# Kernel optimization log

Hardware: AMD Instinct MI355X
Metric: run time of the kernel (lower is better)

The kernel has to match this reference:

```python
import jax, jax.numpy as jnp
import numpy as np

B, S, H, I, E, TOPK = 2, 2048, 1024, 2816, 7, 2


def setup_inputs() -> dict:
    key = jax.random.key(0)
    ks = jax.random.split(key, 8)
    sh = 1.0 / np.sqrt(H).astype(np.float32)   # fan-in scale for H->I projections
    si = 1.0 / np.sqrt(I).astype(np.float32)   # fan-in scale for I->H projections
    return {
        "x": jax.random.normal(ks[0], (B, S, H), jnp.float32),
        "Wg_shared": jax.random.normal(ks[1], (I, H), jnp.float32) * sh,
        "Wu_shared": jax.random.normal(ks[2], (I, H), jnp.float32) * sh,
        "Wd_shared": jax.random.normal(ks[3], (H, I), jnp.float32) * si,
        "Wg": jax.random.normal(ks[4], (E, I, H), jnp.float32) * sh,
        "Wu": jax.random.normal(ks[5], (E, I, H), jnp.float32) * sh,
        "Wd": jax.random.normal(ks[6], (E, H, I), jnp.float32) * si,
        "Wr": jax.random.normal(ks[7], (E, H), jnp.float32) * sh,
    }


def reference(x, Wg_shared, Wu_shared, Wd_shared, Wg, Wu, Wd, Wr):
    # Shared expert: SwiGLU MLP applied to every token.
    sg = jnp.einsum('bsh,ih->bsi', x, Wg_shared)
    su = jnp.einsum('bsh,ih->bsi', x, Wu_shared)
    shared_out = jnp.einsum('bsi,hi->bsh', jax.nn.silu(sg) * su, Wd_shared)

    # Router: top-k over logits, softmax over the selected k logits.
    router_logits = jnp.einsum('bsh,eh->bse', x, Wr)          # [B,S,E]
    rw, sel = jax.lax.top_k(router_logits, TOPK)              # [B,S,K]
    rw = jax.nn.softmax(rw, axis=-1)
    # Per-expert combine weight (equivalent to the scatter-built mask * weight).
    comb = jnp.sum(rw[..., None] * jax.nn.one_hot(sel, E, dtype=x.dtype), axis=2)  # [B,S,E]

    # Torch module runs every expert densely on every token, then masks.
    g = jnp.einsum('bsh,eih->ebsi', x, Wg)                    # [E,B,S,I]
    u = jnp.einsum('bsh,eih->ebsi', x, Wu)
    y = jnp.einsum('ebsi,ehi->ebsh', jax.nn.silu(g) * u, Wd)  # [E,B,S,H]
    moe_out = jnp.einsum('ebsh,bse->bsh', y, comb)

    return shared_out + moe_out, router_logits
```

## Files before the change

kernel.cpp:

```cpp
#include <hip/hip_runtime.h>
#include <hip/hip_bf16.h>

#define NTOK 4096
#define HH 1024
#define II 2816
#define EE 7
#define SHARED_BASE 8192
#define NSLOT 12288

typedef __bf16 bf16x8 __attribute__((ext_vector_type(8)));
typedef __bf16 bf16x4 __attribute__((ext_vector_type(4)));
typedef float  f32x4v __attribute__((ext_vector_type(4)));

__global__ void cvt_x(const float* __restrict__ x, __bf16* __restrict__ xb) {
    int i = blockIdx.x * blockDim.x + threadIdx.x;
    const f32x4v* xv = (const f32x4v*)x;
    bf16x4* ov = (bf16x4*)xb;
    int base = i * 4;
#pragma unroll
    for (int j = 0; j < 4; j++) {
        f32x4v f = xv[base + j];
        bf16x4 b;
        b[0] = (__bf16)f[0]; b[1] = (__bf16)f[1];
        b[2] = (__bf16)f[2]; b[3] = (__bf16)f[3];
        ov[base + j] = b;
    }
}

__global__ void router_k(const float* __restrict__ x, const float* __restrict__ Wr,
                         float* __restrict__ logits, int* __restrict__ counts,
                         int* __restrict__ sel, float* __restrict__ wtop,
                         int* __restrict__ tlist, float* __restrict__ wlist) {
    int wave = threadIdx.x >> 6;
    int lane = threadIdx.x & 63;
    int t = blockIdx.x * 4 + wave;
    const float* xr = x + (size_t)t * HH;
    double acc[EE];
#pragma unroll
    for (int e = 0; e < EE; e++) acc[e] = 0.0;
    for (int j = 0; j < 16; j++) {
        int h = lane + j * 64;
        double xv = (double)xr[h];
#pragma unroll
        for (int e = 0; e < EE; e++) acc[e] += xv * (double)Wr[e * HH + h];
    }
#pragma unroll
    for (int e = 0; e < EE; e++) {
        for (int off = 32; off > 0; off >>= 1) acc[e] += __shfl_down(acc[e], off, 64);
    }
    if (lane == 0) {
        int e0 = 0;
        for (int e = 1; e < EE; e++) if (acc[e] > acc[e0]) e0 = e;
        int e1 = -1;
        for (int e = 0; e < EE; e++) {
            if (e == e0) continue;
            if (e1 < 0 || acc[e] > acc[e1]) e1 = e;
        }
        double w1 = exp(acc[e1] - acc[e0]);
        double s = 1.0 + w1;
        for (int e = 0; e < EE; e++) logits[(size_t)t * EE + e] = (float)acc[e];
        sel[2 * t] = e0; sel[2 * t + 1] = e1;
        wtop[2 * t] = (float)(1.0 / s); wtop[2 * t + 1] = (float)(w1 / s);
        atomicAdd(&counts[e0], 1);
        atomicAdd(&counts[e1], 1);
        tlist[SHARED_BASE + t] = t;
        wlist[SHARED_BASE + t] = 1.0f;
    }
}

__global__ void finalize_k(const int* __restrict__ counts, int* __restrict__ cursor,
                           int* __restrict__ nlist, int* __restrict__ offs) {
    if (threadIdx.x == 0 && blockIdx.x == 0) {
        int o = 0;
        for (int e = 0; e < EE; e++) {
            offs[e] = o; cursor[e] = o; nlist[e] = counts[e];
            o += counts[e];
        }
        offs[EE] = SHARED_BASE;
        nlist[EE] = NTOK;
        cursor[EE] = SHARED_BASE;
    }
}

__global__ void scatter_k(const int* __restrict__ sel, const float* __restrict__ wtop,
                          int* __restrict__ cursor, int* __restrict__ tlist,
                          float* __restrict__ wlist) {
    int t = blockIdx.x * blockDim.x + threadIdx.x;
    if (t >= NTOK) return;
#pragma unroll
    for (int j = 0; j < 2; j++) {
        int e = sel[2 * t + j];
        int slot = atomicAdd(&cursor[e], 1);
        tlist[slot] = t;
        wlist[slot] = wtop[2 * t + j];
    }
}

__global__ __launch_bounds__(256, 3) void gateup_k(
        const float* __restrict__ Wg, const float* __restrict__ Wu,
        const float* __restrict__ Wgs, const float* __restrict__ Wus,
        const __bf16* __restrict__ xb, __bf16* __restrict__ hbuf,
        const int* __restrict__ nlist, const int* __restrict__ offs,
        const int* __restrict__ tlist) {
    const int e = blockIdx.z;
    const int ne = nlist[e];
    const int bx = blockIdx.x;
    const int nt = (bx & 7) + 8 * (bx >> 8);
    const int mt = (bx >> 3) & 31;
    if (nt >= II / 64) return;
    if (mt * 128 >= ne) return;
    const int base = offs[e];
    const float* wg = (e < EE) ? Wg + (size_t)e * II * HH : Wgs;
    const float* wu = (e < EE) ? Wu + (size_t)e * II * HH : Wus;

    __shared__ __bf16 As[128 * 32];
    __shared__ __bf16 Bg[64 * 32];
    __shared__ __bf16 Bu[64 * 32];

    const int tid = threadIdx.x;
    const int arow0 = tid >> 2, c8 = (tid & 3) * 8;
    const int arow1 = arow0 + 64;
    const int cl0 = min(mt * 128 + arow0, ne - 1);
    const int cl1 = min(mt * 128 + arow1, ne - 1);
    const __bf16* aptr0 = xb + (size_t)tlist[base + cl0] * HH + c8;
    const __bf16* aptr1 = xb + (size_t)tlist[base + cl1] * HH + c8;
    const int brow = tid >> 2;
    const size_t boff = (size_t)(nt * 64 + brow) * HH + c8;

    const int wid = tid >> 6, lane = tid & 63;
    const int wm = wid >> 1, wn = wid & 1;
    const int l16 = lane & 15, quad = lane >> 4;

    f32x4v accg[4][2], accu[4][2];
#pragma unroll
    for (int i = 0; i < 4; i++)
#pragma unroll
        for (int j = 0; j < 2; j++) { accg[i][j] = (f32x4v)0.0f; accu[i][j] = (f32x4v)0.0f; }

    bf16x8 aR0 = *(const bf16x8*)aptr0;
    bf16x8 aR1 = *(const bf16x8*)aptr1;
    f32x4v g0 = *(const f32x4v*)(wg + boff);
    f32x4v g1 = *(const f32x4v*)(wg + boff + 4);
    f32x4v u0 = *(const f32x4v*)(wu + boff);
    f32x4v u1 = *(const f32x4v*)(wu + boff + 4);

    for (int k0 = 0; k0 < HH; k0 += 32) {
        bf16x8 bgv, buv;
        bgv[0] = (__bf16)g0[0]; bgv[1] = (__bf16)g0[1]; bgv[2] = (__bf16)g0[2]; bgv[3] = (__bf16)g0[3];
        bgv[4] = (__bf16)g1[0]; bgv[5] = (__bf16)g1[1]; bgv[6] = (__bf16)g1[2]; bgv[7] = (__bf16)g1[3];
        buv[0] = (__bf16)u0[0]; buv[1] = (__bf16)u0[1]; buv[2] = (__bf16)u0[2]; buv[3] = (__bf16)u0[3];
        buv[4] = (__bf16)u1[0]; buv[5] = (__bf16)u1[1]; buv[6] = (__bf16)u1[2]; buv[7] = (__bf16)u1[3];
        __syncthreads();
        *(bf16x8*)&As[arow0 * 32 + c8] = aR0;
        *(bf16x8*)&As[arow1 * 32 + c8] = aR1;
        *(bf16x8*)&Bg[brow * 32 + c8] = bgv;
        *(bf16x8*)&Bu[brow * 32 + c8] = buv;
        if (k0 + 32 < HH) {
            aR0 = *(const bf16x8*)(aptr0 + k0 + 32);
            aR1 = *(const bf16x8*)(aptr1 + k0 + 32);
            g0 = *(const f32x4v*)(wg + boff + k0 + 32);
            g1 = *(const f32x4v*)(wg + boff + k0 + 36);
            u0 = *(const f32x4v*)(wu + boff + k0 + 32);
            u1 = *(const f32x4v*)(wu + boff + k0 + 36);
        }
        __syncthreads();
        bf16x8 a[4];
#pragma unroll
        for (int i = 0; i < 4; i++)
            a[i] = *(const bf16x8*)&As[(wm * 64 + i * 16 + l16) * 32 + quad * 8];
#pragma unroll
        for (int j = 0; j < 2; j++) {
            bf16x8 bg = *(const bf16x8*)&Bg[(wn * 32 + j * 16 + l16) * 32 + quad * 8];
            bf16x8 bu = *(const bf16x8*)&Bu[(wn * 32 + j * 16 + l16) * 32 + quad * 8];
#pragma unroll
            for (int i = 0; i < 4; i++) {
                accg[i][j] = __builtin_amdgcn_mfma_f32_16x16x32_bf16(a[i], bg, accg[i][j], 0, 0, 0);
                accu[i][j] = __builtin_amdgcn_mfma_f32_16x16x32_bf16(a[i], bu, accu[i][j], 0, 0, 0);
            }
        }
    }
#pragma unroll
    for (int i = 0; i < 4; i++) {
        const int mrow = mt * 128 + wm * 64 + i * 16 + quad * 4;
#pragma unroll
        for (int r = 0; r < 4; r++) {
            const int slot = mrow + r;
            if (slot < ne) {
                __bf16* hrow = hbuf + (size_t)(base + slot) * II + nt * 64 + wn * 32 + l16;
#pragma unroll
                for (int j = 0; j < 2; j++) {
                    float g = accg[i][j][r], u = accu[i][j][r];
                    float sgl = g / (1.0f + __expf(-g));
                    hrow[j * 16] = (__bf16)(sgl * u);
                }
            }
        }
    }
}

__global__ __launch_bounds__(256, 3) void down_k(
        const float* __restrict__ Wd, const float* __restrict__ Wds,
        const __bf16* __restrict__ hbuf, float* __restrict__ out,
        const int* __restrict__ nlist, const int* __restrict__ offs,
        const int* __restrict__ tlist, const float* __restrict__ wlist) {
    const int e = blockIdx.z;
    const int ne = nlist[e];
    const int bx = blockIdx.x;
    const int nt = bx & 7;
    const int mt = bx >> 3;
    if (mt * 128 >= ne) return;
    const int base = offs[e];
    const float* wd = (e < EE) ? Wd + (size_t)e * HH * II : Wds;

    __shared__ __bf16 As[128 * 32];
    __shared__ __bf16 Bs[128 * 32];

    const int tid = threadIdx.x;
    const int arow0 = tid >> 2, c8 = (tid & 3) * 8;
    const int arow1 = arow0 + 64;
    const int cl0 = min(mt * 128 + arow0, ne - 1);
    const int cl1 = min(mt * 128 + arow1, ne - 1);
    const __bf16* aptr0 = hbuf + (size_t)(base + cl0) * II + c8;
    const __bf16* aptr1 = hbuf + (size_t)(base + cl1) * II + c8;
    const size_t boff0 = (size_t)(nt * 128 + arow0) * II + c8;
    const size_t boff1 = (size_t)(nt * 128 + arow1) * II + c8;

    const int wid = tid >> 6, lane = tid & 63;
    const int wm = wid >> 1, wn = wid & 1;
    const int l16 = lane & 15, quad = lane >> 4;

    f32x4v acc[4][4];
#pragma unroll
    for (int i = 0; i < 4; i++)
#pragma unroll
        for (int j = 0; j < 4; j++) acc[i][j] = (f32x4v)0.0f;

    bf16x8 aR0 = *(const bf16x8*)aptr0;
    bf16x8 aR1 = *(const bf16x8*)aptr1;
    f32x4v b00 = *(const f32x4v*)(wd + boff0);
    f32x4v b01 = *(const f32x4v*)(wd + boff0 + 4);
    f32x4v b10 = *(const f32x4v*)(wd + boff1);
    f32x4v b11 = *(const f32x4v*)(wd + boff1 + 4);

    for (int k0 = 0; k0 < II; k0 += 32) {
        bf16x8 bs0, bs1;
        bs0[0] = (__bf16)b00[0]; bs0[1] = (__bf16)b00[1]; bs0[2] = (__bf16)b00[2]; bs0[3] = (__bf16)b00[3];
        bs0[4] = (__bf16)b01[0]; bs0[5] = (__bf16)b01[1]; bs0[6] = (__bf16)b01[2]; bs0[7] = (__bf16)b01[3];
        bs1[0] = (__bf16)b10[0]; bs1[1] = (__bf16)b10[1]; bs1[2] = (__bf16)b10[2]; bs1[3] = (__bf16)b10[3];
        bs1[4] = (__bf16)b11[0]; bs1[5] = (__bf16)b11[1]; bs1[6] = (__bf16)b11[2]; bs1[7] = (__bf16)b11[3];
        __syncthreads();
        *(bf16x8*)&As[arow0 * 32 + c8] = aR0;
        *(bf16x8*)&As[arow1 * 32 + c8] = aR1;
        *(bf16x8*)&Bs[arow0 * 32 + c8] = bs0;
        *(bf16x8*)&Bs[arow1 * 32 + c8] = bs1;
        if (k0 + 32 < II) {
            aR0 = *(const bf16x8*)(aptr0 + k0 + 32);
            aR1 = *(const bf16x8*)(aptr1 + k0 + 32);
            b00 = *(const f32x4v*)(wd + boff0 + k0 + 32);
            b01 = *(const f32x4v*)(wd + boff0 + k0 + 36);
            b10 = *(const f32x4v*)(wd + boff1 + k0 + 32);
            b11 = *(const f32x4v*)(wd + boff1 + k0 + 36);
        }
        __syncthreads();
        bf16x8 a[4];
#pragma unroll
        for (int i = 0; i < 4; i++)
            a[i] = *(const bf16x8*)&As[(wm * 64 + i * 16 + l16) * 32 + quad * 8];
#pragma unroll
        for (int j = 0; j < 4; j++) {
            bf16x8 b = *(const bf16x8*)&Bs[(wn * 64 + j * 16 + l16) * 32 + quad * 8];
#pragma unroll
            for (int i = 0; i < 4; i++)
                acc[i][j] = __builtin_amdgcn_mfma_f32_16x16x32_bf16(a[i], b, acc[i][j], 0, 0, 0);
        }
    }
#pragma unroll
    for (int i = 0; i < 4; i++) {
        const int mrow = mt * 128 + wm * 64 + i * 16 + quad * 4;
#pragma unroll
        for (int r = 0; r < 4; r++) {
            const int slot = mrow + r;
            if (slot < ne) {
                const int idx = base + slot;
                const int tok = tlist[idx];
                const float w = wlist[idx];
                float* orow = out + (size_t)tok * HH + nt * 128 + wn * 64 + l16;
#pragma unroll
                for (int j = 0; j < 4; j++)
                    atomicAdd(&orow[j * 16], w * acc[i][j][r]);
            }
        }
    }
}

extern "C" void kernel_launch(void* const* d_in, const int* in_sizes, int n_in,
                              void* d_out, int out_size, void* d_ws, size_t ws_size,
                              hipStream_t stream) {
    const float* x   = (const float*)d_in[0];
    const float* Wgs = (const float*)d_in[1];
    const float* Wus = (const float*)d_in[2];
    const float* Wds = (const float*)d_in[3];
    const float* Wg  = (const float*)d_in[4];
    const float* Wu  = (const float*)d_in[5];
    const float* Wd  = (const float*)d_in[6];
    const float* Wr  = (const float*)d_in[7];
    float* out = (float*)d_out;
    float* logits = out + (size_t)NTOK * HH;

    char* ws = (char*)d_ws;
    __bf16* hbuf = (__bf16*)ws;
    __bf16* xb   = (__bf16*)(ws + (size_t)NSLOT * II * 2);
    char* meta   = ws + (size_t)NSLOT * II * 2 + (size_t)NTOK * HH * 2;
    int* counts = (int*)meta;
    int* cursor = counts + 8;
    int* nlist  = cursor + 8;
    int* offs   = nlist + 8;
    int* sel    = offs + 8;
    int* tlist  = sel + 2 * NTOK;
    float* wtop = (float*)(tlist + NSLOT);
    float* wlist = wtop + 2 * NTOK;

    hipMemsetAsync(counts, 0, 8 * sizeof(int), stream);
    hipMemsetAsync(out, 0, (size_t)NTOK * HH * sizeof(float), stream);

    cvt_x<<<1024, 256, 0, stream>>>(x, xb);
    router_k<<<NTOK / 4, 256, 0, stream>>>(x, Wr, logits, counts, sel, wtop, tlist, wlist);
    finalize_k<<<1, 64, 0, stream>>>(counts, cursor, nlist, offs);
    scatter_k<<<NTOK / 256, 256, 0, stream>>>(sel, wtop, cursor, tlist, wlist);
    gateup_k<<<dim3(1536, 1, EE + 1), 256, 0, stream>>>(Wg, Wu, Wgs, Wus, xb, hbuf,
                                                        nlist, offs, tlist);
    down_k<<<dim3(256, 1, EE + 1), 256, 0, stream>>>(Wd, Wds, hbuf, out,
                                                     nlist, offs, tlist, wlist);
}
```

Before: 821.0 us.

## Pre-convert expert weights to bf16 and stream tiles into LDS directly

Adds a kernel that converts all expert and shared gate, up and down weights from fp32 to bf16 into the workspace on every call. New gate/up and down GEMM kernels then load bf16 tiles straight into swizzled LDS with global_load_lds, skipping per-tile fp32 loads and register conversion. Each weight tile is fetched by many token tiles, so halving its bytes should cut repeated fp32 traffic. The cost is an extra full read and write pass over roughly 280 MB of weights per call, and the fast path runs only when the workspace is large enough, otherwise the old fp32 kernels are used.

```diff
diff --git a/kernel.cpp b/kernel.cpp
--- a/kernel.cpp
+++ b/kernel.cpp
@@ -12,6 +12,12 @@
 typedef __bf16 bf16x4 __attribute__((ext_vector_type(4)));
 typedef float  f32x4v __attribute__((ext_vector_type(4)));
 
+typedef const __attribute__((address_space(1))) void* gas_ptr;
+typedef __attribute__((address_space(3))) void* las_ptr;
+__device__ __forceinline__ void load16_lds(const void* g, void* l) {
+    __builtin_amdgcn_global_load_lds((gas_ptr)g, (las_ptr)l, 16, 0, 0);
+}
+
 __global__ void cvt_x(const float* __restrict__ x, __bf16* __restrict__ xb) {
     int i = blockIdx.x * blockDim.x + threadIdx.x;
     const f32x4v* xv = (const f32x4v*)x;
@@ -24,6 +30,32 @@
         b[0] = (__bf16)f[0]; b[1] = (__bf16)f[1];
         b[2] = (__bf16)f[2]; b[3] = (__bf16)f[3];
         ov[base + j] = b;
+    }
+}
+
+__global__ void cvt_w6(const float* __restrict__ s0, const float* __restrict__ s1,
+                       const float* __restrict__ s2, const float* __restrict__ s3,
+                       const float* __restrict__ s4, const float* __restrict__ s5,
+                       __bf16* __restrict__ d0, __bf16* __restrict__ d1,
+                       __bf16* __restrict__ d2, __bf16* __restrict__ d3,
+                       __bf16* __restrict__ d4, __bf16* __restrict__ d5) {
+    const int y = blockIdx.y;
+    const float* s; __bf16* d; int n4;
+    if (y == 0)      { s = s0; d = d0; n4 = (EE * II * HH) / 4; }
+    else if (y == 1) { s = s1; d = d1; n4 = (EE * II * HH) / 4; }
+    else if (y == 2) { s = s2; d = d2; n4 = (EE * II * HH) / 4; }
+    else if (y == 3) { s = s3; d = d3; n4 = (II * HH) / 4; }
+    else if (y == 4) { s = s4; d = d4; n4 = (II * HH) / 4; }
+    else             { s = s5; d = d5; n4 = (II * HH) / 4; }
+    const f32x4v* sv = (const f32x4v*)s;
+    bf16x4* dv = (bf16x4*)d;
+    for (int i = blockIdx.x * blockDim.x + threadIdx.x; i < n4;
+         i += gridDim.x * blockDim.x) {
+        f32x4v f = sv[i];
+        bf16x4 b;
+        b[0] = (__bf16)f[0]; b[1] = (__bf16)f[1];
+        b[2] = (__bf16)f[2]; b[3] = (__bf16)f[3];
+        dv[i] = b;
     }
 }
 
@@ -96,7 +128,176 @@
     }
 }
 
-__global__ __launch_bounds__(256, 3) void gateup_k(
+__global__ __launch_bounds__(256, 3) void gateup_bf(
+        const __bf16* __restrict__ Wg, const __bf16* __restrict__ Wu,
+        const __bf16* __restrict__ Wgs, const __bf16* __restrict__ Wus,
+        const __bf16* __restrict__ xb, __bf16* __restrict__ hbuf,
+        const int* __restrict__ nlist, const int* __restrict__ offs,
+        const int* __restrict__ tlist) {
+    const int e = blockIdx.z;
+    const int ne = nlist[e];
+    const int bx = blockIdx.x;
+    const int nt = (bx & 7) + 8 * (bx >> 8);
+    const int mt = (bx >> 3) & 31;
+    if (nt >= II / 64) return;
+    if (mt * 128 >= ne) return;
+    const int base = offs[e];
+    const __bf16* wg = (e < EE) ? Wg + (size_t)e * II * HH : Wgs;
+    const __bf16* wu = (e < EE) ? Wu + (size_t)e * II * HH : Wus;
+
+    __shared__ __bf16 As[128 * 32];
+    __shared__ __bf16 Bg[64 * 32];
+    __shared__ __bf16 Bu[64 * 32];
+
+    const int tid = threadIdx.x;
+    const int r0 = tid >> 2;
+    const int c  = tid & 3;
+    const int cs = (c ^ ((r0 >> 1) & 3)) * 8;
+    const int cl0 = min(mt * 128 + r0, ne - 1);
+    const int cl1 = min(mt * 128 + r0 + 64, ne - 1);
+    const __bf16* aptr0 = xb + (size_t)tlist[base + cl0] * HH + cs;
+    const __bf16* aptr1 = xb + (size_t)tlist[base + cl1] * HH + cs;
+    const __bf16* bgp = wg + (size_t)(nt * 64 + r0) * HH + cs;
+    const __bf16* bup = wu + (size_t)(nt * 64 + r0) * HH + cs;
+    __bf16* ldsA0 = &As[tid * 8];
+    __bf16* ldsA1 = &As[64 * 32 + tid * 8];
+    __bf16* ldsBg = &Bg[tid * 8];
+    __bf16* ldsBu = &Bu[tid * 8];
+
+    const int wid = tid >> 6, lane = tid & 63;
+    const int wm = wid >> 1, wn = wid & 1;
+    const int l16 = lane & 15, quad = lane >> 4;
+    const int qsw = (quad ^ ((l16 >> 1) & 3)) * 8;
+
+    f32x4v accg[4][2], accu[4][2];
+#pragma unroll
+    for (int i = 0; i < 4; i++)
+#pragma unroll
+        for (int j = 0; j < 2; j++) { accg[i][j] = (f32x4v)0.0f; accu[i][j] = (f32x4v)0.0f; }
+
+    for (int k0 = 0; k0 < HH; k0 += 32) {
+        __syncthreads();
+        load16_lds(aptr0 + k0, ldsA0);
+        load16_lds(aptr1 + k0, ldsA1);
+        load16_lds(bgp + k0, ldsBg);
+        load16_lds(bup + k0, ldsBu);
+        __syncthreads();
+        bf16x8 a[4];
+#pragma unroll
+        for (int i = 0; i < 4; i++)
+            a[i] = *(const bf16x8*)&As[(wm * 64 + i * 16 + l16) * 32 + qsw];
+#pragma unroll
+        for (int j = 0; j < 2; j++) {
+            bf16x8 bg = *(const bf16x8*)&Bg[(wn * 32 + j * 16 + l16) * 32 + qsw];
+            bf16x8 bu = *(const bf16x8*)&Bu[(wn * 32 + j * 16 + l16) * 32 + qsw];
+#pragma unroll
+            for (int i = 0; i < 4; i++) {
+                accg[i][j] = __builtin_amdgcn_mfma_f32_16x16x32_bf16(a[i], bg, accg[i][j], 0, 0, 0);
+                accu[i][j] = __builtin_amdgcn_mfma_f32_16x16x32_bf16(a[i], bu, accu[i][j], 0, 0, 0);
+            }
+        }
+    }
+#pragma unroll
+    for (int i = 0; i < 4; i++) {
+        const int mrow = mt * 128 + wm * 64 + i * 16 + quad * 4;
+#pragma unroll
+        for (int r = 0; r < 4; r++) {
+            const int slot = mrow + r;
+            if (slot < ne) {
+                __bf16* hrow = hbuf + (size_t)(base + slot) * II + nt * 64 + wn * 32 + l16;
+#pragma unroll
+                for (int j = 0; j < 2; j++) {
+                    float g = accg[i][j][r], u = accu[i][j][r];
+                    float sgl = g / (1.0f + __expf(-g));
+                    hrow[j * 16] = (__bf16)(sgl * u);
+                }
+            }
+        }
+    }
+}
+
+__global__ __launch_bounds__(256, 3) void down_bf(
+        const __bf16* __restrict__ Wd, const __bf16* __restrict__ Wds,
+        const __bf16* __restrict__ hbuf, float* __restrict__ out,
+        const int* __restrict__ nlist, const int* __restrict__ offs,
+        const int* __restrict__ tlist, const float* __restrict__ wlist) {
+    const int e = blockIdx.z;
+    const int ne = nlist[e];
+    const int bx = blockIdx.x;
+    const int nt = bx & 7;
+    const int mt = bx >> 3;
+    if (mt * 128 >= ne) return;
+    const int base = offs[e];
+    const __bf16* wd = (e < EE) ? Wd + (size_t)e * HH * II : Wds;
+
+    __shared__ __bf16 As[128 * 32];
+    __shared__ __bf16 Bs[128 * 32];
+
+    const int tid = threadIdx.x;
+    const int r0 = tid >> 2;
+    const int c  = tid & 3;
+    const int cs = (c ^ ((r0 >> 1) & 3)) * 8;
+    const int cl0 = min(mt * 128 + r0, ne - 1);
+    const int cl1 = min(mt * 128 + r0 + 64, ne - 1);
+    const __bf16* aptr0 = hbuf + (size_t)(base + cl0) * II + cs;
+    const __bf16* aptr1 = hbuf + (size_t)(base + cl1) * II + cs;
+    const __bf16* bptr0 = wd + (size_t)(nt * 128 + r0) * II + cs;
+    const __bf16* bptr1 = wd + (size_t)(nt * 128 + r0 + 64) * II + cs;
+    __bf16* ldsA0 = &As[tid * 8];
+    __bf16* ldsA1 = &As[64 * 32 + tid * 8];
+    __bf16* ldsB0 = &Bs[tid * 8];
+    __bf16* ldsB1 = &Bs[64 * 32 + tid * 8];
+
+    const int wid = tid >> 6, lane = tid & 63;
+    const int wm = wid >> 1, wn = wid & 1;
+    const int l16 = lane & 15, quad = lane >> 4;
+    const int qsw = (quad ^ ((l16 >> 1) & 3)) * 8;
+
+    f32x4v acc[4][4];
+#pragma unroll
+    for (int i = 0; i < 4; i++)
+#pragma unroll
+        for (int j = 0; j < 4; j++) acc[i][j] = (f32x4v)0.0f;
+
+    for (int k0 = 0; k0 < II; k0 += 32) {
+        __syncthreads();
+        load16_lds(aptr0 + k0, ldsA0);
+        load16_lds(aptr1 + k0, ldsA1);
+        load16_lds(bptr0 + k0, ldsB0);
+        load16_lds(bptr1 + k0, ldsB1);
+        __syncthreads();
+        bf16x8 a[4];
+#pragma unroll
+        for (int i = 0; i < 4; i++)
+            a[i] = *(const bf16x8*)&As[(wm * 64 + i * 16 + l16) * 32 + qsw];
+#pragma unroll
+        for (int j = 0; j < 4; j++) {
+            bf16x8 b = *(const bf16x8*)&Bs[(wn * 64 + j * 16 + l16) * 32 + qsw];
+#pragma unroll
+            for (int i = 0; i < 4; i++)
+                acc[i][j] = __builtin_amdgcn_mfma_f32_16x16x32_bf16(a[i], b, acc[i][j], 0, 0, 0);
+        }
+    }
+#pragma unroll
+    for (int i = 0; i < 4; i++) {
+        const int mrow = mt * 128 + wm * 64 + i * 16 + quad * 4;
+#pragma unroll
+        for (int r = 0; r < 4; r++) {
+            const int slot = mrow + r;
+            if (slot < ne) {
+                const int idx = base + slot;
+                const int tok = tlist[idx];
+                const float w = wlist[idx];
+                float* orow = out + (size_t)tok * HH + nt * 128 + wn * 64 + l16;
+#pragma unroll
+                for (int j = 0; j < 4; j++)
+                    atomicAdd(&orow[j * 16], w * acc[i][j][r]);
+            }
+        }
+    }
+}
+
+__global__ __launch_bounds__(256, 3) void gateup_f32(
         const float* __restrict__ Wg, const float* __restrict__ Wu,
         const float* __restrict__ Wgs, const float* __restrict__ Wus,
         const __bf16* __restrict__ xb, __bf16* __restrict__ hbuf,
@@ -198,7 +399,7 @@
     }
 }
 
-__global__ __launch_bounds__(256, 3) void down_k(
+__global__ __launch_bounds__(256, 3) void down_f32(
         const float* __restrict__ Wd, const float* __restrict__ Wds,
         const __bf16* __restrict__ hbuf, float* __restrict__ out,
         const int* __restrict__ nlist, const int* __restrict__ offs,
@@ -307,28 +508,70 @@
     float* out = (float*)d_out;
     float* logits = out + (size_t)NTOK * HH;
 
+    const size_t HB  = (size_t)NSLOT * II * 2;
+    const size_t XB  = (size_t)NTOK * HH * 2;
+    const size_t WEB = (size_t)EE * II * HH * 2;
+    const size_t WSB = (size_t)II * HH * 2;
+    const size_t META = 262144;
+    const size_t needFast = HB + XB + 3 * WEB + 3 * WSB + META;
+
     char* ws = (char*)d_ws;
-    __bf16* hbuf = (__bf16*)ws;
-    __bf16* xb   = (__bf16*)(ws + (size_t)NSLOT * II * 2);
-    char* meta   = ws + (size_t)NSLOT * II * 2 + (size_t)NTOK * HH * 2;
-    int* counts = (int*)meta;
-    int* cursor = counts + 8;
-    int* nlist  = cursor + 8;
-    int* offs   = nlist + 8;
-    int* sel    = offs + 8;
-    int* tlist  = sel + 2 * NTOK;
-    float* wtop = (float*)(tlist + NSLOT);
-    float* wlist = wtop + 2 * NTOK;
-
-    hipMemsetAsync(counts, 0, 8 * sizeof(int), stream);
-    hipMemsetAsync(out, 0, (size_t)NTOK * HH * sizeof(float), stream);
-
-    cvt_x<<<1024, 256, 0, stream>>>(x, xb);
-    router_k<<<NTOK / 4, 256, 0, stream>>>(x, Wr, logits, counts, sel, wtop, tlist, wlist);
-    finalize_k<<<1, 64, 0, stream>>>(counts, cursor, nlist, offs);
-    scatter_k<<<NTOK / 256, 256, 0, stream>>>(sel, wtop, cursor, tlist, wlist);
-    gateup_k<<<dim3(1536, 1, EE + 1), 256, 0, stream>>>(Wg, Wu, Wgs, Wus, xb, hbuf,
-                                                        nlist, offs, tlist);
-    down_k<<<dim3(256, 1, EE + 1), 256, 0, stream>>>(Wd, Wds, hbuf, out,
-                                                     nlist, offs, tlist, wlist);
-}
+
+    if (ws_size >= needFast) {
+        __bf16* hbuf = (__bf16*)ws;
+        __bf16* xb   = (__bf16*)(ws + HB);
+        __bf16* wgb  = (__bf16*)(ws + HB + XB);
+        __bf16* wub  = (__bf16*)(ws + HB + XB + WEB);
+        __bf16* wdb  = (__bf16*)(ws + HB + XB + 2 * WEB);
+        __bf16* wgsb = (__bf16*)(ws + HB + XB + 3 * WEB);
+        __bf16* wusb = (__bf16*)(ws + HB + XB + 3 * WEB + WSB);
+        __bf16* wdsb = (__bf16*)(ws + HB + XB + 3 * WEB + 2 * WSB);
+        char* meta   = ws + HB + XB + 3 * WEB + 3 * WSB;
+        int* counts = (int*)meta;
+        int* cursor = counts + 8;
+        int* nlist  = cursor + 8;
+        int* offs   = nlist + 8;
+        int* sel    = offs + 8;
+        int* tlist  = sel + 2 * NTOK;
+        float* wtop = (float*)(tlist + NSLOT);
+        float* wlist = wtop + 2 * NTOK;
+
+        hipMemsetAsync(counts, 0, 8 * sizeof(int), stream);
+        hipMemsetAsync(out, 0, (size_t)NTOK * HH * sizeof(float), stream);
+
+        cvt_x<<<1024, 256, 0, stream>>>(x, xb);
+        cvt_w6<<<dim3(1024, 6), 256, 0, stream>>>(Wg, Wu, Wd, Wgs, Wus, Wds,
+                                                  wgb, wub, wdb, wgsb, wusb, wdsb);
+        router_k<<<NTOK / 4, 256, 0, stream>>>(x, Wr, logits, counts, sel, wtop, tlist, wlist);
+        finalize_k<<<1, 64, 0, stream>>>(counts, cursor, nlist, offs);
+        scatter_k<<<NTOK / 256, 256, 0, stream>>>(sel, wtop, cursor, tlist, wlist);
+        gateup_bf<<<dim3(1536, 1, EE + 1), 256, 0, stream>>>(wgb, wub, wgsb, wusb, xb, hbuf,
+                                                             nlist, offs, tlist);
+        down_bf<<<dim3(256, 1, EE + 1), 256, 0, stream>>>(wdb, wdsb, hbuf, out,
+                                                          nlist, offs, tlist, wlist);
+    } else {
+        __bf16* hbuf = (__bf16*)ws;
+        __bf16* xb   = (__bf16*)(ws + HB);
+        char* meta   = ws + HB + XB;
+        int* counts = (int*)meta;
+        int* cursor = counts + 8;
+        int* nlist  = cursor + 8;
+        int* offs   = nlist + 8;
+        int* sel    = offs + 8;
+        int* tlist  = sel + 2 * NTOK;
+        float* wtop = (float*)(tlist + NSLOT);
+        float* wlist = wtop + 2 * NTOK;
+
+        hipMemsetAsync(counts, 0, 8 * sizeof(int), stream);
+        hipMemsetAsync(out, 0, (size_t)NTOK * HH * sizeof(float), stream);
+
+        cvt_x<<<1024, 256, 0, stream>>>(x, xb);
+        router_k<<<NTOK / 4, 256, 0, stream>>>(x, Wr, logits, counts, sel, wtop, tlist, wlist);
+        finalize_k<<<1, 64, 0, stream>>>(counts, cursor, nlist, offs);
+        scatter_k<<<NTOK / 256, 256, 0, stream>>>(sel, wtop, cursor, tlist, wlist);
+        gateup_f32<<<dim3(1536, 1, EE + 1), 256, 0, stream>>>(Wg, Wu, Wgs, Wus, xb, hbuf,
+                                                              nlist, offs, tlist);
+        down_f32<<<dim3(256, 1, EE + 1), 256, 0, stream>>>(Wd, Wds, hbuf, out,
+                                                           nlist, offs, tlist, wlist);
+    }
+}
```

Result: faster. 773.1 us (-5.8%).
